# Performance work log

Measured on AMD Instinct MI355X. Metric: run time of the kernel, lower is better.

## Reference

```python
import jax, jax.numpy as jnp
import numpy as np

IN_FEATURES = 4096
OUT_FEATURES = 4096
MIN_BLOCK = 64
RANK = 16
NUM_LAYERS = 6  # log2(4096 / 64)
BATCH, SEQ = 4, 4096


def _perm(i, out_features):
    # permutations[i] = arange(out).reshape(2**i, 2, -1)[:, (1, 0), :].flatten()
    return np.arange(out_features).reshape(2 ** i, 2, -1)[:, ::-1, :].reshape(-1)


def setup_inputs() -> dict:
    key = jax.random.key(0)
    ks = jax.random.split(key, 2 * NUM_LAYERS + 3)
    inp = {}
    inp["x"] = jax.random.normal(ks[0], (BATCH, SEQ, IN_FEATURES), dtype=jnp.float32)
    for i in range(NUM_LAYERS):
        n = 2 ** (i + 1)
        r = min(RANK, IN_FEATURES // n)
        inp[f"us{i}"] = jax.random.normal(ks[1 + i], (n, IN_FEATURES // n, r), dtype=jnp.float32) * 0.02
        inp[f"vs{i}"] = jax.random.normal(ks[1 + NUM_LAYERS + i], (n, r, OUT_FEATURES // n), dtype=jnp.float32) * 0.02
    m = 2 ** NUM_LAYERS
    inp["ds"] = jax.random.normal(ks[-2], (m, IN_FEATURES // m, OUT_FEATURES // m), dtype=jnp.float32) * 0.02
    inp["bias"] = jax.random.normal(ks[-1], (OUT_FEATURES,), dtype=jnp.float32) * 0.02
    return inp


def reference(x, us0, us1, us2, us3, us4, us5,
              vs0, vs1, vs2, vs3, vs4, vs5, ds, bias):
    us = [us0, us1, us2, us3, us4, us5]
    vs = [vs0, vs1, vs2, vs3, vs4, vs5]
    *dims, d_in = x.shape
    out_features = ds.shape[0] * ds.shape[2]
    output = jnp.zeros((*dims, out_features), dtype=x.dtype)
    for i in range(len(us)):
        n = 2 ** (i + 1)
        xb = x.reshape(*dims, n, d_in // n)          # (..., n, d_in/n)
        # low-rank off-diagonal contribution: (..., n, d_out/n)
        val = jnp.einsum('...ni,nij,njk->...nk', xb, us[i], vs[i]).reshape(*dims, -1)
        output = output.at[..., _perm(i, out_features)].add(val)
    m = ds.shape[0]
    diag = jnp.einsum('...ni,nij->...nj', x.reshape(*dims, m, d_in // m), ds)
    output = output + diag.reshape(*dims, out_features)
    return output + bias
```

## Files before the change

kernel.cpp:

```cpp
#include <hip/hip_runtime.h>

#define D 4096
#define CSTRIDE 2016

typedef unsigned short u16;
typedef __bf16 bf16x8 __attribute__((ext_vector_type(8)));
typedef u16    u16x8  __attribute__((ext_vector_type(8)));
typedef u16    u16x4v __attribute__((ext_vector_type(4)));
typedef float  f32x4  __attribute__((ext_vector_type(4)));

__device__ __forceinline__ u16 f2bf(float f) {
    unsigned u = __float_as_uint(f);
    u += 0x7fffu + ((u >> 16) & 1u);
    return (u16)(u >> 16);
}

__global__ __launch_bounds__(256) void hodlr_prep(
    const float* __restrict__ us0, const float* __restrict__ us1,
    const float* __restrict__ us2, const float* __restrict__ us3,
    const float* __restrict__ us4, const float* __restrict__ us5,
    const float* __restrict__ vs0, const float* __restrict__ vs1,
    const float* __restrict__ vs2, const float* __restrict__ vs3,
    const float* __restrict__ vs4, const float* __restrict__ vs5,
    const float* __restrict__ dsm,
    u16* __restrict__ usT, u16* __restrict__ WT)
{
    const float* usp[6] = {us0, us1, us2, us3, us4, us5};
    const float* vsp[6] = {vs0, vs1, vs2, vs3, vs4, vs5};
    const int idx = blockIdx.x * 256 + threadIdx.x;
    if (idx < 6 * 65536) {
        const int i = idx >> 16, rem = idx & 65535;
        const int lg = 11 - i, s = 2048 >> i;
        const int jr = rem >> lg, k = rem & (s - 1);
        const int j = jr >> 4, r = jr & 15;
        usT[idx] = f2bf(usp[i][(size_t)(j * s + k) * 16 + r]);
    } else if (idx < 6 * 65536 + 64 * 10240) {
        const int w = idx - 6 * 65536;
        const int b = w / 10240, rem = w - b * 10240;
        const int n = rem / 160, k = rem - n * 160;
        float val;
        if (k < 64) {
            val = dsm[b * 4096 + k * 64 + n];
        } else {
            const int i = (k - 64) >> 4, r = (k - 64) & 15;
            const int s = 2048 >> i;
            const int sib = (b >> (5 - i)) ^ 1;
            const int loc = b & ((1 << (5 - i)) - 1);
            val = vsp[i][(size_t)sib * 16 * s + r * s + loc * 64 + n];
        }
        WT[w] = f2bf(val);
    }
}

__global__ __launch_bounds__(256) void hodlr_codes(
    const float* __restrict__ x, const u16* __restrict__ usT,
    u16* __restrict__ codes)
{
    __shared__ __align__(16) u16 uss[6 * 16 * 72];

    const int tid = threadIdx.x, lane = tid & 63, wv = tid >> 6;
    const int m = lane & 15, quad = lane >> 4;
    const int t0 = blockIdx.x * 64;
    const int kbase = blockIdx.y * 2048;
    const float* xrow = x + (size_t)(t0 + wv * 16 + m) * D;

    f32x4 acc[6];
    #pragma unroll
    for (int i = 0; i < 6; ++i) acc[i] = (f32x4){0.f, 0.f, 0.f, 0.f};

    for (int c = 0; c < 32; ++c) {
        const int kb = kbase + c * 64;
        __syncthreads();
        const float4 xv0 = *(const float4*)(xrow + kb + quad * 8);
        const float4 xv1 = *(const float4*)(xrow + kb + quad * 8 + 4);
        const float4 xv2 = *(const float4*)(xrow + kb + 32 + quad * 8);
        const float4 xv3 = *(const float4*)(xrow + kb + 32 + quad * 8 + 4);
        #pragma unroll
        for (int p = 0; p < 3; ++p) {
            const int u = tid + p * 256;
            const int i = u >> 7, rem = u & 127, r = rem >> 3, seg = rem & 7;
            const int lg = 11 - i;
            const int j = kb >> lg;
            const int koff = kb & ((2048 >> i) - 1);
            const size_t src = ((size_t)i << 16) + ((size_t)((j << 4) + r) << lg)
                             + koff + (seg << 3);
            *(float4*)&uss[(i * 16 + r) * 72 + (seg << 3)] =
                *(const float4*)(usT + src);
        }
        __syncthreads();

        union { u16x8 u; bf16x8 v; } a0, a1;
        a0.u[0] = f2bf(xv0.x); a0.u[1] = f2bf(xv0.y); a0.u[2] = f2bf(xv0.z); a0.u[3] = f2bf(xv0.w);
        a0.u[4] = f2bf(xv1.x); a0.u[5] = f2bf(xv1.y); a0.u[6] = f2bf(xv1.z); a0.u[7] = f2bf(xv1.w);
        a1.u[0] = f2bf(xv2.x); a1.u[1] = f2bf(xv2.y); a1.u[2] = f2bf(xv2.z); a1.u[3] = f2bf(xv2.w);
        a1.u[4] = f2bf(xv3.x); a1.u[5] = f2bf(xv3.y); a1.u[6] = f2bf(xv3.z); a1.u[7] = f2bf(xv3.w);

        #pragma unroll
        for (int i = 0; i < 6; ++i) {
            const u16* bp = &uss[(i * 16 + m) * 72 + quad * 8];
            const bf16x8 b0 = *(const bf16x8*)bp;
            const bf16x8 b1 = *(const bf16x8*)(bp + 32);
            acc[i] = __builtin_amdgcn_mfma_f32_16x16x32_bf16(a0.v, b0, acc[i], 0, 0, 0);
            acc[i] = __builtin_amdgcn_mfma_f32_16x16x32_bf16(a1.v, b1, acc[i], 0, 0, 0);
        }
        #pragma unroll
        for (int i = 0; i < 6; ++i) {
            const int s = 2048 >> i;
            if (((kb + 64) & (s - 1)) == 0) {
                const int j = kb >> (11 - i);
                const int offt = 16 * ((2 << i) - 2);
                u16* cp = codes + (size_t)(t0 + wv * 16 + quad * 4) * CSTRIDE
                        + offt + j * 16 + m;
                cp[0 * CSTRIDE] = f2bf(acc[i][0]);
                cp[1 * CSTRIDE] = f2bf(acc[i][1]);
                cp[2 * CSTRIDE] = f2bf(acc[i][2]);
                cp[3 * CSTRIDE] = f2bf(acc[i][3]);
                acc[i] = (f32x4){0.f, 0.f, 0.f, 0.f};
            }
        }
    }
}

__global__ __launch_bounds__(256) void hodlr_out(
    const float* __restrict__ x, const u16* __restrict__ codes,
    const u16* __restrict__ WT, const float* __restrict__ bias,
    float* __restrict__ out)
{
    __shared__ __align__(16) u16 As[64 * 168];
    __shared__ __align__(16) u16 Ws[64 * 168];

    const int tid = threadIdx.x, lane = tid & 63, wv = tid >> 6;
    const int m = lane & 15, quad = lane >> 4;
    const int bch = blockIdx.x, t0 = blockIdx.y * 64;

    #pragma unroll
    for (int p = 0; p < 4; ++p) {
        const int idx = tid + p * 256;
        const int row = idx >> 4, c4 = idx & 15;
        const float4 xv = *(const float4*)(x + (size_t)(t0 + row) * D + bch * 64 + c4 * 4);
        u16x4v pk; pk[0] = f2bf(xv.x); pk[1] = f2bf(xv.y); pk[2] = f2bf(xv.z); pk[3] = f2bf(xv.w);
        *(u16x4v*)&As[row * 168 + c4 * 4] = pk;
    }
    #pragma unroll
    for (int p = 0; p < 3; ++p) {
        const int u = tid + p * 256;
        const int row = u / 12, rem = u - row * 12, i = rem >> 1, h = rem & 1;
        const int offt = 16 * ((2 << i) - 2);
        const int sib = (bch >> (5 - i)) ^ 1;
        *(float4*)&As[row * 168 + 64 + i * 16 + h * 8] =
            *(const float4*)(codes + (size_t)(t0 + row) * CSTRIDE + offt + sib * 16 + h * 8);
    }
    #pragma unroll
    for (int p = 0; p < 5; ++p) {
        const int u = tid + p * 256;
        const int n = u / 20, seg = u - n * 20;
        *(float4*)&Ws[n * 168 + seg * 8] =
            *(const float4*)(WT + (size_t)bch * 10240 + (size_t)u * 8);
    }
    __syncthreads();

    f32x4 acc[4];
    #pragma unroll
    for (int nt = 0; nt < 4; ++nt) acc[nt] = (f32x4){0.f, 0.f, 0.f, 0.f};

    #pragma unroll
    for (int s = 0; s < 5; ++s) {
        const bf16x8 a = *(const bf16x8*)&As[(wv * 16 + m) * 168 + s * 32 + quad * 8];
        #pragma unroll
        for (int nt = 0; nt < 4; ++nt) {
            const bf16x8 b = *(const bf16x8*)&Ws[(nt * 16 + m) * 168 + s * 32 + quad * 8];
            acc[nt] = __builtin_amdgcn_mfma_f32_16x16x32_bf16(a, b, acc[nt], 0, 0, 0);
        }
    }
    __syncthreads();

    float* Of = (float*)As;
    #pragma unroll
    for (int nt = 0; nt < 4; ++nt)
        #pragma unroll
        for (int v = 0; v < 4; ++v)
            Of[(wv * 16 + quad * 4 + v) * 68 + nt * 16 + m] = acc[nt][v];
    __syncthreads();

    #pragma unroll
    for (int p = 0; p < 4; ++p) {
        const int u = tid + p * 256;
        const int row = u >> 4, seg = u & 15;
        float4 val = *(const float4*)&Of[row * 68 + seg * 4];
        const float4 bv = *(const float4*)(bias + bch * 64 + seg * 4);
        val.x += bv.x; val.y += bv.y; val.z += bv.z; val.w += bv.w;
        *(float4*)(out + (size_t)(t0 + row) * D + bch * 64 + seg * 4) = val;
    }
}

extern "C" void kernel_launch(void* const* d_in, const int* in_sizes, int n_in,
                              void* d_out, int out_size, void* d_ws, size_t ws_size,
                              hipStream_t stream)
{
    const float* x   = (const float*)d_in[0];
    const float* us0 = (const float*)d_in[1];
    const float* vs0 = (const float*)d_in[2];
    const float* us1 = (const float*)d_in[3];
    const float* vs1 = (const float*)d_in[4];
    const float* us2 = (const float*)d_in[5];
    const float* vs2 = (const float*)d_in[6];
    const float* us3 = (const float*)d_in[7];
    const float* vs3 = (const float*)d_in[8];
    const float* us4 = (const float*)d_in[9];
    const float* vs4 = (const float*)d_in[10];
    const float* us5 = (const float*)d_in[11];
    const float* vs5 = (const float*)d_in[12];
    const float* dsm = (const float*)d_in[13];
    const float* bias= (const float*)d_in[14];
    float* out = (float*)d_out;

    const int T = in_sizes[0] / D;

    u16* codes = (u16*)d_ws;
    u16* usT   = codes + (size_t)T * CSTRIDE;
    u16* WTp   = usT + 6 * 65536;

    hipLaunchKernelGGL(hodlr_prep, dim3((6 * 65536 + 64 * 10240) / 256), dim3(256), 0, stream,
                       us0, us1, us2, us3, us4, us5,
                       vs0, vs1, vs2, vs3, vs4, vs5, dsm, usT, WTp);
    hipLaunchKernelGGL(hodlr_codes, dim3(T / 64, 2), dim3(256), 0, stream,
                       x, usT, codes);
    hipLaunchKernelGGL(hodlr_out, dim3(64, T / 64), dim3(256), 0, stream,
                       x, codes, WTp, bias, out);
}
```

Before: 629.7 us.

## Double-buffer shared U tiles and prefetch next chunk into registers in codes kernel

The codes kernel now uses two shared-memory buffers for the U tiles and loads the next chunk's U and x values into registers while the current chunk is computed. This drops one of the two barriers per iteration and lets global-load latency overlap the MFMA work. Per-thread shared-memory offsets are hoisted out of the loop, and the loop is unrolled by four. The cost is more registers and twice the shared memory. The single barrier plus alternating buffers must still be enough to prevent write-after-read races.

```diff
diff --git a/kernel.cpp b/kernel.cpp
--- a/kernel.cpp
+++ b/kernel.cpp
@@ -56,7 +56,7 @@
     const float* __restrict__ x, const u16* __restrict__ usT,
     u16* __restrict__ codes)
 {
-    __shared__ __align__(16) u16 uss[6 * 16 * 72];
+    __shared__ __align__(16) u16 uss[2][6 * 16 * 72];
 
     const int tid = threadIdx.x, lane = tid & 63, wv = tid >> 6;
     const int m = lane & 15, quad = lane >> 4;
@@ -64,30 +64,45 @@
     const int kbase = blockIdx.y * 2048;
     const float* xrow = x + (size_t)(t0 + wv * 16 + m) * D;
 
+    int sOff[3], sI[3], sR[3], sSeg[3];
+    #pragma unroll
+    for (int p = 0; p < 3; ++p) {
+        const int u = tid + p * 256;
+        const int i = u >> 7, rem = u & 127, r = rem >> 3, seg = rem & 7;
+        sI[p] = i; sR[p] = r; sSeg[p] = seg;
+        sOff[p] = (i * 16 + r) * 72 + (seg << 3);
+    }
+
+    auto usrc = [&](int p, int kb) -> const float4* {
+        const int i = sI[p], lg = 11 - i;
+        const size_t src = ((size_t)i << 16)
+            + ((size_t)(((kb >> lg) << 4) + sR[p]) << lg)
+            + (size_t)(kb & ((2048 >> i) - 1)) + (sSeg[p] << 3);
+        return (const float4*)(usT + src);
+    };
+
     f32x4 acc[6];
     #pragma unroll
     for (int i = 0; i < 6; ++i) acc[i] = (f32x4){0.f, 0.f, 0.f, 0.f};
 
+    float4 uv0, uv1, uv2, xv0, xv1, xv2, xv3;
+    {
+        const int kb = kbase;
+        uv0 = *usrc(0, kb); uv1 = *usrc(1, kb); uv2 = *usrc(2, kb);
+        xv0 = *(const float4*)(xrow + kb + quad * 8);
+        xv1 = *(const float4*)(xrow + kb + quad * 8 + 4);
+        xv2 = *(const float4*)(xrow + kb + 32 + quad * 8);
+        xv3 = *(const float4*)(xrow + kb + 32 + quad * 8 + 4);
+    }
+
+    #pragma unroll 4
     for (int c = 0; c < 32; ++c) {
         const int kb = kbase + c * 64;
-        __syncthreads();
-        const float4 xv0 = *(const float4*)(xrow + kb + quad * 8);
-        const float4 xv1 = *(const float4*)(xrow + kb + quad * 8 + 4);
-        const float4 xv2 = *(const float4*)(xrow + kb + 32 + quad * 8);
-        const float4 xv3 = *(const float4*)(xrow + kb + 32 + quad * 8 + 4);
-        #pragma unroll
-        for (int p = 0; p < 3; ++p) {
-            const int u = tid + p * 256;
-            const int i = u >> 7, rem = u & 127, r = rem >> 3, seg = rem & 7;
-            const int lg = 11 - i;
-            const int j = kb >> lg;
-            const int koff = kb & ((2048 >> i) - 1);
-            const size_t src = ((size_t)i << 16) + ((size_t)((j << 4) + r) << lg)
-                             + koff + (seg << 3);
-            *(float4*)&uss[(i * 16 + r) * 72 + (seg << 3)] =
-                *(const float4*)(usT + src);
-        }
-        __syncthreads();
+        u16* ubuf = uss[c & 1];
+
+        *(float4*)&ubuf[sOff[0]] = uv0;
+        *(float4*)&ubuf[sOff[1]] = uv1;
+        *(float4*)&ubuf[sOff[2]] = uv2;
 
         union { u16x8 u; bf16x8 v; } a0, a1;
         a0.u[0] = f2bf(xv0.x); a0.u[1] = f2bf(xv0.y); a0.u[2] = f2bf(xv0.z); a0.u[3] = f2bf(xv0.w);
@@ -95,14 +110,28 @@
         a1.u[0] = f2bf(xv2.x); a1.u[1] = f2bf(xv2.y); a1.u[2] = f2bf(xv2.z); a1.u[3] = f2bf(xv2.w);
         a1.u[4] = f2bf(xv3.x); a1.u[5] = f2bf(xv3.y); a1.u[6] = f2bf(xv3.z); a1.u[7] = f2bf(xv3.w);
 
+        if (c < 31) {
+            const int kn = kb + 64;
+            uv0 = *usrc(0, kn); uv1 = *usrc(1, kn); uv2 = *usrc(2, kn);
+            xv0 = *(const float4*)(xrow + kn + quad * 8);
+            xv1 = *(const float4*)(xrow + kn + quad * 8 + 4);
+            xv2 = *(const float4*)(xrow + kn + 32 + quad * 8);
+            xv3 = *(const float4*)(xrow + kn + 32 + quad * 8 + 4);
+        }
+
+        asm volatile("s_waitcnt lgkmcnt(0)" ::: "memory");
+        __builtin_amdgcn_s_barrier();
+        asm volatile("" ::: "memory");
+
         #pragma unroll
         for (int i = 0; i < 6; ++i) {
-            const u16* bp = &uss[(i * 16 + m) * 72 + quad * 8];
+            const u16* bp = &ubuf[(i * 16 + m) * 72 + quad * 8];
             const bf16x8 b0 = *(const bf16x8*)bp;
             const bf16x8 b1 = *(const bf16x8*)(bp + 32);
             acc[i] = __builtin_amdgcn_mfma_f32_16x16x32_bf16(a0.v, b0, acc[i], 0, 0, 0);
             acc[i] = __builtin_amdgcn_mfma_f32_16x16x32_bf16(a1.v, b1, acc[i], 0, 0, 0);
         }
+
         #pragma unroll
         for (int i = 0; i < 6; ++i) {
             const int s = 2048 >> i;
```

Result: no change. 632.4 us (+0.4%).

## Split codes kernel K dimension into eight segments with partial-sum reduction

Applied to the files above, without the earlier changes.

The codes kernel now splits the input dimension into eight 512-wide segments instead of two 2048-wide halves, which multiplies the grid by four to raise occupancy. Levels 0 and 1, whose spans cover more than one segment, write fp32 partial sums to a workspace buffer. A new small reduce kernel sums those partials and writes bf16 codes. This adds an extra launch and partial-sum traffic in exchange for more parallelism in the x-streaming pass, and the launch bounds now request 8 blocks per CU.

```diff
diff --git a/kernel.cpp b/kernel.cpp
--- a/kernel.cpp
+++ b/kernel.cpp
@@ -52,23 +52,24 @@
     }
 }
 
-__global__ __launch_bounds__(256) void hodlr_codes(
+__global__ __launch_bounds__(256, 8) void hodlr_codes(
     const float* __restrict__ x, const u16* __restrict__ usT,
-    u16* __restrict__ codes)
+    u16* __restrict__ codes, float* __restrict__ part)
 {
     __shared__ __align__(16) u16 uss[6 * 16 * 72];
 
     const int tid = threadIdx.x, lane = tid & 63, wv = tid >> 6;
     const int m = lane & 15, quad = lane >> 4;
     const int t0 = blockIdx.x * 64;
-    const int kbase = blockIdx.y * 2048;
+    const int seg = blockIdx.y;
+    const int kbase = seg * 512;
     const float* xrow = x + (size_t)(t0 + wv * 16 + m) * D;
 
     f32x4 acc[6];
     #pragma unroll
     for (int i = 0; i < 6; ++i) acc[i] = (f32x4){0.f, 0.f, 0.f, 0.f};
 
-    for (int c = 0; c < 32; ++c) {
+    for (int c = 0; c < 8; ++c) {
         const int kb = kbase + c * 64;
         __syncthreads();
         const float4 xv0 = *(const float4*)(xrow + kb + quad * 8);
@@ -78,13 +79,13 @@
         #pragma unroll
         for (int p = 0; p < 3; ++p) {
             const int u = tid + p * 256;
-            const int i = u >> 7, rem = u & 127, r = rem >> 3, seg = rem & 7;
+            const int i = u >> 7, rem = u & 127, r = rem >> 3, sg = rem & 7;
             const int lg = 11 - i;
             const int j = kb >> lg;
             const int koff = kb & ((2048 >> i) - 1);
             const size_t src = ((size_t)i << 16) + ((size_t)((j << 4) + r) << lg)
-                             + koff + (seg << 3);
-            *(float4*)&uss[(i * 16 + r) * 72 + (seg << 3)] =
+                             + koff + (sg << 3);
+            *(float4*)&uss[(i * 16 + r) * 72 + (sg << 3)] =
                 *(const float4*)(usT + src);
         }
         __syncthreads();
@@ -104,7 +105,7 @@
             acc[i] = __builtin_amdgcn_mfma_f32_16x16x32_bf16(a1.v, b1, acc[i], 0, 0, 0);
         }
         #pragma unroll
-        for (int i = 0; i < 6; ++i) {
+        for (int i = 2; i < 6; ++i) {
             const int s = 2048 >> i;
             if (((kb + 64) & (s - 1)) == 0) {
                 const int j = kb >> (11 - i);
@@ -119,6 +120,35 @@
             }
         }
     }
+
+    const int prow = t0 + wv * 16 + quad * 4;
+    float* pp = part + ((size_t)prow * 8 + seg) * 32 + m;
+    #pragma unroll
+    for (int v = 0; v < 4; ++v) {
+        pp[(size_t)v * 256]      = acc[0][v];
+        pp[(size_t)v * 256 + 16] = acc[1][v];
+    }
+}
+
+__global__ __launch_bounds__(256) void hodlr_reduce(
+    const float* __restrict__ part, u16* __restrict__ codes)
+{
+    const int idx = blockIdx.x * 256 + threadIdx.x;
+    const int row = idx / 96, rem = idx - row * 96;
+    float s;
+    int off;
+    if (rem < 32) {
+        const int j = rem >> 4, r = rem & 15;
+        const float* p = part + ((size_t)row * 8 + j * 4) * 32 + r;
+        s = (p[0] + p[32]) + (p[64] + p[96]);
+        off = j * 16 + r;
+    } else {
+        const int rm = rem - 32, j = rm >> 4, r = rm & 15;
+        const float* p = part + ((size_t)row * 8 + j * 2) * 32 + 16 + r;
+        s = p[0] + p[32];
+        off = 32 + j * 16 + r;
+    }
+    codes[(size_t)row * CSTRIDE + off] = f2bf(s);
 }
 
 __global__ __launch_bounds__(256) void hodlr_out(
@@ -153,8 +183,8 @@
     #pragma unroll
     for (int p = 0; p < 5; ++p) {
         const int u = tid + p * 256;
-        const int n = u / 20, seg = u - n * 20;
-        *(float4*)&Ws[n * 168 + seg * 8] =
+        const int n = u / 20, sg = u - n * 20;
+        *(float4*)&Ws[n * 168 + sg * 8] =
             *(const float4*)(WT + (size_t)bch * 10240 + (size_t)u * 8);
     }
     __syncthreads();
@@ -185,11 +215,11 @@
     #pragma unroll
     for (int p = 0; p < 4; ++p) {
         const int u = tid + p * 256;
-        const int row = u >> 4, seg = u & 15;
-        float4 val = *(const float4*)&Of[row * 68 + seg * 4];
-        const float4 bv = *(const float4*)(bias + bch * 64 + seg * 4);
+        const int row = u >> 4, sg = u & 15;
+        float4 val = *(const float4*)&Of[row * 68 + sg * 4];
+        const float4 bv = *(const float4*)(bias + bch * 64 + sg * 4);
         val.x += bv.x; val.y += bv.y; val.z += bv.z; val.w += bv.w;
-        *(float4*)(out + (size_t)(t0 + row) * D + bch * 64 + seg * 4) = val;
+        *(float4*)(out + (size_t)(t0 + row) * D + bch * 64 + sg * 4) = val;
     }
 }
 
@@ -219,12 +249,15 @@
     u16* codes = (u16*)d_ws;
     u16* usT   = codes + (size_t)T * CSTRIDE;
     u16* WTp   = usT + 6 * 65536;
+    float* part = (float*)(WTp + 64 * 10240);
 
     hipLaunchKernelGGL(hodlr_prep, dim3((6 * 65536 + 64 * 10240) / 256), dim3(256), 0, stream,
                        us0, us1, us2, us3, us4, us5,
                        vs0, vs1, vs2, vs3, vs4, vs5, dsm, usT, WTp);
-    hipLaunchKernelGGL(hodlr_codes, dim3(T / 64, 2), dim3(256), 0, stream,
-                       x, usT, codes);
+    hipLaunchKernelGGL(hodlr_codes, dim3(T / 64, 8), dim3(256), 0, stream,
+                       x, usT, codes, part);
+    hipLaunchKernelGGL(hodlr_reduce, dim3(T * 96 / 256), dim3(256), 0, stream,
+                       part, codes);
     hipLaunchKernelGGL(hodlr_out, dim3(64, T / 64), dim3(256), 0, stream,
                        x, codes, WTp, bias, out);
 }
```

Measured after the change: 638.5 us. No clear change (+1.4%).
